# Optimization experiments

Hardware: AMD Instinct MI355X
Metric: run time of the kernel (lower is better)

## Reference

```python
import jax, jax.numpy as jnp
import numpy as np

N_GENE, N_PATH, N_VACC = 50000, 20000, 10000
N_TOT = N_GENE + N_PATH + N_VACC
HID = 128
E_PER = 250000
K_APPNP = 8
ALPHA = 0.1
N_LAYERS = 2


def setup_inputs() -> dict:
    key = jax.random.key(0)
    ks = iter(jax.random.split(key, 40))
    f32 = jnp.float32

    def nrm(shape, scale=1.0):
        return jax.random.normal(next(ks), shape, dtype=f32) * scale

    def edges(n_src, n_dst):
        src = jax.random.randint(next(ks), (E_PER,), 0, n_src)
        dst = jax.random.randint(next(ks), (E_PER,), 0, n_dst)
        return jnp.stack([src, dst]).astype(jnp.int32)

    return {
        "x_gene": nrm((N_GENE, 256)),
        "x_pathway": nrm((N_PATH, 128)),
        "x_vaccine": nrm((N_VACC, 64)),
        "win_gene": nrm((HID, 256), 256 ** -0.5),
        "bin_gene": jnp.zeros((HID,), f32),
        "win_pathway": nrm((HID, 128), 128 ** -0.5),
        "bin_pathway": jnp.zeros((HID,), f32),
        "win_vaccine": nrm((HID, 64), 64 ** -0.5),
        "bin_vaccine": jnp.zeros((HID,), f32),
        "w_sage_l": nrm((N_LAYERS, 4, HID, HID), HID ** -0.5),
        "b_sage_l": jnp.zeros((N_LAYERS, 4, HID), f32),
        "w_sage_r": nrm((N_LAYERS, 4, HID, HID), HID ** -0.5),
        "ei_targets": edges(N_VACC, N_GENE),    # vaccine -> gene
        "ei_in": edges(N_GENE, N_PATH),         # gene -> pathway
        "ei_contains": edges(N_PATH, N_GENE),   # pathway -> gene
        "ei_interacts": edges(N_GENE, N_GENE),  # gene -> gene
    }


def _sage(x_src, x_dst, ei, wl, bl, wr, n_dst):
    # PyG SAGEConv(aggr='mean'): lin_l(mean_j x_src[j]) + lin_r(x_dst); bias lives in lin_l
    src, dst = ei[0], ei[1]
    s = jax.ops.segment_sum(x_src[src], dst, num_segments=n_dst)
    cnt = jax.ops.segment_sum(jnp.ones((ei.shape[1],), x_src.dtype), dst, num_segments=n_dst)
    agg = s / jnp.maximum(cnt, 1.0)[:, None]  # isolated dst nodes -> 0
    return agg @ wl.T + bl + x_dst @ wr.T


def _forward(x_gene, x_pathway, x_vaccine, win_gene, bin_gene, win_pathway, bin_pathway,
             win_vaccine, bin_vaccine, w_sage_l, b_sage_l, w_sage_r,
             ei_targets, ei_in, ei_contains, ei_interacts):
    # input projections + relu
    hg = jax.nn.relu(x_gene @ win_gene.T + bin_gene)
    hp = jax.nn.relu(x_pathway @ win_pathway.T + bin_pathway)
    hv = jax.nn.relu(x_vaccine @ win_vaccine.T + bin_vaccine)
    # hetero SAGE layers with residual + relu (dropout: eval mode -> identity)
    for l in range(N_LAYERS):
        o_tg = _sage(hv, hg, ei_targets, w_sage_l[l, 0], b_sage_l[l, 0], w_sage_r[l, 0], N_GENE)
        o_in = _sage(hg, hp, ei_in, w_sage_l[l, 1], b_sage_l[l, 1], w_sage_r[l, 1], N_PATH)
        o_ct = _sage(hp, hg, ei_contains, w_sage_l[l, 2], b_sage_l[l, 2], w_sage_r[l, 2], N_GENE)
        o_ii = _sage(hg, hg, ei_interacts, w_sage_l[l, 3], b_sage_l[l, 3], w_sage_r[l, 3], N_GENE)
        hg = jax.nn.relu(hg + (o_tg + o_ct + o_ii) / 3.0)  # HeteroConv aggr='mean' over 3 relations
        hp = jax.nn.relu(hp + o_in)
        hv = jax.nn.relu(hv)  # no incoming relation -> zero message
    # APPNP on homogeneous graph; node order = [gene | pathway | vaccine]
    OG, OP, OV = 0, N_GENE, N_GENE + N_PATH
    loops = jnp.arange(N_TOT, dtype=jnp.int32)
    row = jnp.concatenate([ei_targets[0] + OV, ei_in[0] + OG, ei_contains[0] + OP, ei_interacts[0] + OG, loops])
    col = jnp.concatenate([ei_targets[1] + OG, ei_in[1] + OP, ei_contains[1] + OG, ei_interacts[1] + OG, loops])
    deg = jax.ops.segment_sum(jnp.ones(row.shape, hg.dtype), col, num_segments=N_TOT)
    dinv = jnp.where(deg > 0, deg ** -0.5, 0.0)
    norm = (dinv[row] * dinv[col])[:, None]
    h0 = jnp.concatenate([hg, hp, hv], axis=0)  # [N_TOT, HID]

    def step(z, _):
        m = jax.ops.segment_sum(norm * z[row], col, num_segments=N_TOT)
        return (1.0 - ALPHA) * m + ALPHA * h0, None

    z, _ = jax.lax.scan(step, h0, None, length=K_APPNP)
    return z  # [N_TOT, HID]; rows 0:50000 gene, 50000:70000 pathway, 70000:80000 vaccine


def reference(x_gene, x_pathway, x_vaccine, win_gene, bin_gene, win_pathway, bin_pathway,
              win_vaccine, bin_vaccine, w_sage_l, b_sage_l, w_sage_r,
              ei_targets, ei_in, ei_contains, ei_interacts):
    return _forward(x_gene, x_pathway, x_vaccine, win_gene, bin_gene, win_pathway, bin_pathway,
                    win_vaccine, bin_vaccine, w_sage_l, b_sage_l, w_sage_r,
                    ei_targets, ei_in, ei_contains, ei_interacts)
```

## Files before the change

### kernel.cpp

```cpp
#include <hip/hip_runtime.h>

#define N_GENE 50000
#define N_PATH 20000
#define N_VACC 10000
#define N_TOT  80000
#define HID    128
#define E_PER  250000
#define OG 0
#define OP 50000
#define OV 70000

typedef _Float16  f16x8  __attribute__((ext_vector_type(8)));
typedef _Float16  f16x4  __attribute__((ext_vector_type(4)));
typedef float     f32x4  __attribute__((ext_vector_type(4)));

__constant__ int c_segn[4] = {N_GENE, N_PATH, N_GENE, N_GENE};
__constant__ int c_segb[4] = {0, 50000, 70000, 120000};
#define CNT_TOTAL 170000

struct Off4 { int* p[4]; };
struct CntSeg { const int* dst; int* cnt; };
struct Cnt4 { CntSeg s[4]; };
struct F4Seg { const int* ei; const int* off; int* rows; int2* pk; int soff; };
struct F4 { F4Seg s[4]; };
struct AggSeg { const int* rows; const int* off; _Float16* out; int ldo; int n; };
struct Agg4 { AggSeg s[4]; };
struct CsrP { const int* off; const int2* pk; };


__global__ void count4_kernel(Cnt4 a, int* __restrict__ rank)
{
    int seg = blockIdx.y;
    int e = blockIdx.x * 256 + threadIdx.x;
    if (e < E_PER) rank[seg * E_PER + e] = atomicAdd(&a.s[seg].cnt[a.s[seg].dst[e]], 1);
}

__global__ void scan1_kernel(const int* __restrict__ cnt, int* __restrict__ partials)
{
    int seg = blockIdx.y, blk = blockIdx.x;
    int n = c_segn[seg];
    if (blk >= ((n + 4095) >> 12)) return;
    const int* base = cnt + c_segb[seg];
    int t = threadIdx.x;
    int i0 = (blk << 12) + t * 16;
    int s = 0;
#pragma unroll
    for (int j = 0; j < 16; j++) { int i = i0 + j; if (i < n) s += base[i]; }
    __shared__ int sh[256];
    sh[t] = s; __syncthreads();
    for (int d = 128; d; d >>= 1) { if (t < d) sh[t] += sh[t + d]; __syncthreads(); }
    if (t == 0) partials[seg * 32 + blk] = sh[0];
}

__global__ void scan2_kernel(int* __restrict__ partials, Off4 offs)
{
    int s = threadIdx.x;
    if (s < 4) {
        int n = c_segn[s];
        int nb = (n + 4095) >> 12;
        int run = 0;
        for (int b = 0; b < nb; b++) { int v = partials[s * 32 + b]; partials[s * 32 + b] = run; run += v; }
        offs.p[s][n] = run;
    }
}

__global__ void scan3_kernel(const int* __restrict__ cnt, const int* __restrict__ partials, Off4 offs)
{
    int seg = blockIdx.y, blk = blockIdx.x;
    int n = c_segn[seg];
    if (blk >= ((n + 4095) >> 12)) return;
    const int* base = cnt + c_segb[seg];
    int* off = offs.p[seg];
    int t = threadIdx.x;
    int i0 = (blk << 12) + t * 16;
    int loc[16];
    int s = 0;
#pragma unroll
    for (int j = 0; j < 16; j++) { int i = i0 + j; int v = (i < n) ? base[i] : 0; loc[j] = s; s += v; }
    __shared__ int sh[256];
    sh[t] = s; __syncthreads();
    for (int d = 1; d < 256; d <<= 1) {
        int v = (t >= d) ? sh[t - d] : 0; __syncthreads();
        sh[t] += v; __syncthreads();
    }
    int base_off = sh[t] - s + partials[seg * 32 + blk];
#pragma unroll
    for (int j = 0; j < 16; j++) { int i = i0 + j; if (i < n) off[i] = base_off + loc[j]; }
}

__global__ void dinv_kernel(const int* __restrict__ r0, const int* __restrict__ r1,
                            const int* __restrict__ r2, const int* __restrict__ r3,
                            float* __restrict__ dinv)
{
    int i = blockIdx.x * 256 + threadIdx.x;
    if (i >= N_TOT) return;
    int deg = 1;
    if (i < N_GENE) deg += (r0[i + 1] - r0[i]) + (r2[i + 1] - r2[i]) + (r3[i + 1] - r3[i]);
    else if (i < OV) { int k = i - OP; deg += r1[k + 1] - r1[k]; }
    dinv[i] = rsqrtf((float)deg);
}

__global__ void fill4_kernel(F4 a, const int* __restrict__ rank, const float* __restrict__ dinv)
{
    int seg = blockIdx.y;
    int e = blockIdx.x * 256 + threadIdx.x;
    if (e >= E_PER) return;
    const int* ei = a.s[seg].ei;
    int s = ei[e] + a.s[seg].soff;
    int d = ei[E_PER + e];
    int pos = a.s[seg].off[d] + rank[seg * E_PER + e];
    a.s[seg].rows[pos] = s;
    if (a.s[seg].pk) a.s[seg].pk[pos] = make_int2(s, __float_as_int(dinv[s]));
}


__global__ void agg_all_kernel(Agg4 a, const _Float16* __restrict__ Hh)
{
    int seg = blockIdx.y;
    int t = threadIdx.x;
    int node = blockIdx.x * 16 + (t >> 4);
    if (node >= a.s[seg].n) return;
    const int* rows = a.s[seg].rows;
    int sub = t & 15;
    int s = a.s[seg].off[node], e = a.s[seg].off[node + 1];
    float acc0[8] = {}, acc1[8] = {};
    int i = s;
    for (; i + 4 <= e; i += 4) {
        int r0 = rows[i], r1 = rows[i + 1], r2 = rows[i + 2], r3 = rows[i + 3];
        f16x8 x0 = *(const f16x8*)&Hh[(size_t)r0 * HID + sub * 8];
        f16x8 x1 = *(const f16x8*)&Hh[(size_t)r1 * HID + sub * 8];
        f16x8 x2 = *(const f16x8*)&Hh[(size_t)r2 * HID + sub * 8];
        f16x8 x3 = *(const f16x8*)&Hh[(size_t)r3 * HID + sub * 8];
#pragma unroll
        for (int j = 0; j < 8; j++) {
            acc0[j] += (float)x0[j] + (float)x1[j];
            acc1[j] += (float)x2[j] + (float)x3[j];
        }
    }
    for (; i < e; i++) {
        f16x8 x = *(const f16x8*)&Hh[(size_t)rows[i] * HID + sub * 8];
#pragma unroll
        for (int j = 0; j < 8; j++) acc0[j] += (float)x[j];
    }
    float inv = (e > s) ? 1.0f / (float)(e - s) : 0.0f;
    f16x8 o;
#pragma unroll
    for (int j = 0; j < 8; j++) o[j] = (_Float16)((acc0[j] + acc1[j]) * inv);
    *(f16x8*)&a.s[seg].out[(size_t)node * a.s[seg].ldo + sub * 8] = o;
}

__global__ void base_kernel(const _Float16* __restrict__ Hh, const int* __restrict__ r0rows,
                            const int* __restrict__ r0off, const float* __restrict__ dinv,
                            _Float16* __restrict__ base, _Float16* __restrict__ z0,
                            float* __restrict__ dout)
{
    int t = threadIdx.x;
    int node = blockIdx.x * 16 + (t >> 4);
    int sub = t & 15;
    size_t idx = (size_t)node * HID + sub * 8;
    f16x8 h = *(const f16x8*)&Hh[idx];
    if (node >= OV) {
        f32x4 o0, o1;
#pragma unroll
        for (int j = 0; j < 4; j++) { o0[j] = (float)h[j]; o1[j] = (float)h[j + 4]; }
        *(f32x4*)&dout[idx] = o0;
        *(f32x4*)&dout[idx + 4] = o1;
        return;
    }
    float acc[8] = {};
    if (node < N_GENE) {
        for (int i = r0off[node]; i < r0off[node + 1]; i++) {
            f16x8 v = *(const f16x8*)&Hh[(size_t)r0rows[i] * HID + sub * 8];
#pragma unroll
            for (int j = 0; j < 8; j++) acc[j] += (float)v[j];
        }
        float sc = 0.9f * dinv[node];
#pragma unroll
        for (int j = 0; j < 8; j++) acc[j] *= sc;
    }
    f16x8 bo;
#pragma unroll
    for (int j = 0; j < 8; j++) bo[j] = (_Float16)(0.1f * (float)h[j] + acc[j]);
    *(f16x8*)&base[idx] = bo;
    *(f16x8*)&z0[idx] = h;
}

__device__ __forceinline__ void gathp(const int* __restrict__ off, const int2* __restrict__ pk,
                                      int node, int sub, const _Float16* __restrict__ zin,
                                      float (&A0)[8], float (&A1)[8])
{
    int s = off[node], e = off[node + 1];
    int i = s;
    for (; i + 4 <= e; i += 4) {
        int2 p0 = pk[i], p1 = pk[i + 1], p2 = pk[i + 2], p3 = pk[i + 3];
        f16x8 x0 = *(const f16x8*)&zin[(size_t)p0.x * HID + sub * 8];
        f16x8 x1 = *(const f16x8*)&zin[(size_t)p1.x * HID + sub * 8];
        f16x8 x2 = *(const f16x8*)&zin[(size_t)p2.x * HID + sub * 8];
        f16x8 x3 = *(const f16x8*)&zin[(size_t)p3.x * HID + sub * 8];
        float w0 = __int_as_float(p0.y), w1 = __int_as_float(p1.y);
        float w2 = __int_as_float(p2.y), w3 = __int_as_float(p3.y);
#pragma unroll
        for (int j = 0; j < 8; j++) {
            A0[j] += (float)x0[j] * w0 + (float)x1[j] * w1;
            A1[j] += (float)x2[j] * w2 + (float)x3[j] * w3;
        }
    }
    for (; i < e; i++) {
        int2 p = pk[i];
        float w = __int_as_float(p.y);
        f16x8 x = *(const f16x8*)&zin[(size_t)p.x * HID + sub * 8];
#pragma unroll
        for (int j = 0; j < 8; j++) A0[j] += (float)x[j] * w;
    }
}

template<typename OT>
__launch_bounds__(256)
__global__ void appnp_kernel(const _Float16* __restrict__ zin, OT* __restrict__ zout,
                             const _Float16* __restrict__ base,
                             CsrP c1, CsrP c2, CsrP c3, const float* __restrict__ dinv)
{
    int t = threadIdx.x;
    int c = blockIdx.x * 16 + (t >> 4);
    int sub = t & 15;
    float A0[8] = {}, A1[8] = {};
    if (c < OP) {
        gathp(c2.off, c2.pk, c, sub, zin, A0, A1);
        gathp(c3.off, c3.pk, c, sub, zin, A0, A1);
    } else {
        gathp(c1.off, c1.pk, c - OP, sub, zin, A0, A1);
    }
    float dc = dinv[c];
    float d2 = dc * dc;
    size_t idx = (size_t)c * HID + sub * 8;
    f16x8 zi = *(const f16x8*)&zin[idx];
    f16x8 bs = *(const f16x8*)&base[idx];
    float res[8];
#pragma unroll
    for (int j = 0; j < 8; j++)
        res[j] = 0.9f * (dc * (A0[j] + A1[j]) + d2 * (float)zi[j]) + (float)bs[j];
    if constexpr (sizeof(OT) == 2) {
        f16x8 o;
#pragma unroll
        for (int j = 0; j < 8; j++) o[j] = (_Float16)res[j];
        *(f16x8*)&zout[idx] = o;
    } else {
        f32x4 o0, o1;
#pragma unroll
        for (int j = 0; j < 4; j++) { o0[j] = res[j]; o1[j] = res[j + 4]; }
        *(f32x4*)&zout[idx] = o0;
        *(f32x4*)&zout[idx + 4] = o1;
    }
}


__global__ void prep_all_kernel(const float* __restrict__ wg, const float* __restrict__ wp,
                                const float* __restrict__ wv,
                                _Float16* __restrict__ obg, _Float16* __restrict__ obp, _Float16* __restrict__ obv,
                                const float* __restrict__ wsl, const float* __restrict__ bsl,
                                const float* __restrict__ wsr,
                                _Float16* __restrict__ Wg0, _Float16* __restrict__ Wg1,
                                _Float16* __restrict__ Wp0, _Float16* __restrict__ Wp1,
                                float* __restrict__ bg0, float* __restrict__ bg1,
                                float* __restrict__ bp0, float* __restrict__ bp1)
{
    int y = blockIdx.y;
    int i = blockIdx.x * 256 + threadIdx.x;
    if (y == 0) {
        if (i < 32768) obg[i] = (_Float16)wg[i];
        if (i < 16384) obp[i] = (_Float16)wp[i];
        if (i < 8192)  obv[i] = (_Float16)wv[i];
        return;
    }
    int layer = y - 1;
    const float* WL = wsl + (size_t)layer * 4 * HID * HID;
    const float* WR = wsr + (size_t)layer * 4 * HID * HID;
    _Float16* Wg = layer ? Wg1 : Wg0;
    _Float16* Wp = layer ? Wp1 : Wp0;
    float* bg = layer ? bg1 : bg0;
    float* bp = layer ? bp1 : bp0;
    if (i < 128 * 512) {
        int nr = i >> 9, k = i & 511;
        float v;
        if (k < 128)      v = WL[0 * 16384 + nr * 128 + k];
        else if (k < 256) v = WL[2 * 16384 + nr * 128 + (k - 128)];
        else if (k < 384) v = WL[3 * 16384 + nr * 128 + (k - 256)];
        else {
            int kk = k - 384;
            v = WR[0 * 16384 + nr * 128 + kk] + WR[2 * 16384 + nr * 128 + kk] + WR[3 * 16384 + nr * 128 + kk];
        }
        Wg[i] = (_Float16)v;
    }
    if (i < 128 * 256) {
        int nr = i >> 8, k = i & 255;
        float v = (k < 128) ? WL[1 * 16384 + nr * 128 + k] : WR[1 * 16384 + nr * 128 + (k - 128)];
        Wp[i] = (_Float16)v;
    }
    if (i < 128) {
        const float* BL = bsl + (size_t)layer * 4 * HID;
        bg[i] = BL[0 * 128 + i] + BL[2 * 128 + i] + BL[3 * 128 + i];
        bp[i] = BL[1 * 128 + i];
    }
}


template<int KT, int K1, bool A_F32, bool SAGE>
__launch_bounds__(256)
__global__ void tgemm_kernel(const void* __restrict__ A1_, const _Float16* __restrict__ A2,
                             const _Float16* __restrict__ W, const float* __restrict__ bias,
                             float scale, _Float16* __restrict__ Hh, int M)
{
    __shared__ _Float16 lds[128 * 40];
    int t = threadIdx.x;
    int wave = t >> 6, lane = t & 63;
    int r = lane & 15, quad = lane >> 4;
    int mbase = blockIdx.x * 128 + wave * 32;
    int mm0 = min(mbase + r, M - 1);
    int mm1 = min(mbase + 16 + r, M - 1);
    const float* Af = (const float*)A1_;
    const _Float16* Ab = (const _Float16*)A1_;

    f32x4 acc[2][8];
#pragma unroll
    for (int s = 0; s < 2; s++)
#pragma unroll
        for (int n = 0; n < 8; n++) acc[s][n] = (f32x4){0.f, 0.f, 0.f, 0.f};

    int srow = t >> 1;
    int selt = (t & 1) * 16;

#pragma unroll
    for (int k0 = 0; k0 < KT; k0 += 32) {
        __syncthreads();
        {
            const _Float16* wsrc = W + (size_t)srow * KT + k0 + selt;
            f16x8 w0 = *(const f16x8*)wsrc;
            f16x8 w1 = *(const f16x8*)(wsrc + 8);
            *(f16x8*)&lds[srow * 40 + selt] = w0;
            *(f16x8*)&lds[srow * 40 + selt + 8] = w1;
        }
        f16x8 a0, a1;
        if constexpr (A_F32) {
            const float* p0 = Af + (size_t)mm0 * KT + k0 + quad * 8;
            const float* p1 = Af + (size_t)mm1 * KT + k0 + quad * 8;
            f32x4 x0 = *(const f32x4*)p0, x1 = *(const f32x4*)(p0 + 4);
            f32x4 y0 = *(const f32x4*)p1, y1 = *(const f32x4*)(p1 + 4);
#pragma unroll
            for (int j = 0; j < 4; j++) { a0[j] = (_Float16)x0[j]; a0[j + 4] = (_Float16)x1[j]; }
#pragma unroll
            for (int j = 0; j < 4; j++) { a1[j] = (_Float16)y0[j]; a1[j + 4] = (_Float16)y1[j]; }
        } else if (k0 < K1) {
            a0 = *(const f16x8*)(Ab + (size_t)mm0 * K1 + k0 + quad * 8);
            a1 = *(const f16x8*)(Ab + (size_t)mm1 * K1 + k0 + quad * 8);
        } else {
            a0 = *(const f16x8*)(A2 + (size_t)mm0 * 128 + (k0 - K1) + quad * 8);
            a1 = *(const f16x8*)(A2 + (size_t)mm1 * 128 + (k0 - K1) + quad * 8);
        }
        __syncthreads();
#pragma unroll
        for (int nt = 0; nt < 8; nt++) {
            f16x8 b = *(const f16x8*)&lds[(nt * 16 + r) * 40 + quad * 8];
            acc[0][nt] = __builtin_amdgcn_mfma_f32_16x16x32_f16(a0, b, acc[0][nt], 0, 0, 0);
            acc[1][nt] = __builtin_amdgcn_mfma_f32_16x16x32_f16(a1, b, acc[1][nt], 0, 0, 0);
        }
    }

#pragma unroll
    for (int sub = 0; sub < 2; sub++) {
#pragma unroll
        for (int nt = 0; nt < 8; nt++) {
            int n = nt * 16 + r;
            float bv = bias[n];
#pragma unroll
            for (int i = 0; i < 4; i++) {
                int row = mbase + sub * 16 + quad * 4 + i;
                if (row >= M) continue;
                size_t idx = (size_t)row * HID + n;
                float v;
                if constexpr (SAGE) v = fmaxf((float)Hh[idx] + (acc[sub][nt][i] + bv) * scale, 0.f);
                else                v = fmaxf(acc[sub][nt][i] + bv, 0.f);
                Hh[idx] = (_Float16)v;
            }
        }
    }
}


extern "C" void kernel_launch(void* const* d_in, const int* in_sizes, int n_in,
                              void* d_out, int out_size, void* d_ws, size_t ws_size,
                              hipStream_t stream)
{
    (void)in_sizes; (void)n_in; (void)out_size; (void)ws_size;

    const float* x_gene = (const float*)d_in[0];
    const float* x_path = (const float*)d_in[1];
    const float* x_vacc = (const float*)d_in[2];
    const float* win_g  = (const float*)d_in[3];
    const float* bin_g  = (const float*)d_in[4];
    const float* win_p  = (const float*)d_in[5];
    const float* bin_p  = (const float*)d_in[6];
    const float* win_v  = (const float*)d_in[7];
    const float* bin_v  = (const float*)d_in[8];
    const float* wsl    = (const float*)d_in[9];
    const float* bsl    = (const float*)d_in[10];
    const float* wsr    = (const float*)d_in[11];
    const int* ei_tg  = (const int*)d_in[12];
    const int* ei_ing = (const int*)d_in[13];
    const int* ei_ct  = (const int*)d_in[14];
    const int* ei_ii  = (const int*)d_in[15];

    char* p = (char*)d_ws;
    auto alloc = [&](size_t b) { char* r = p; p += (b + 255) & ~((size_t)255); return r; };

    _Float16* Hh   = (_Float16*)alloc((size_t)N_TOT * HID * 2);
    _Float16* BASE = (_Float16*)alloc((size_t)OV * HID * 2);
    _Float16* Z1   = (_Float16*)alloc((size_t)OV * HID * 2);
    _Float16* Z2   = (_Float16*)alloc((size_t)OV * HID * 2);
    _Float16* AGG_G = (_Float16*)alloc((size_t)N_GENE * 384 * 2);
    _Float16* AGG_P = (_Float16*)alloc((size_t)N_PATH * 128 * 2);
    float* dinv   = (float*)alloc((size_t)N_TOT * 4);
    int* r_rows[4], *r_off[4];
    for (int r = 0; r < 4; r++) r_rows[r] = (int*)alloc((size_t)E_PER * 4);
    r_off[0] = (int*)alloc((size_t)(N_GENE + 1) * 4);
    r_off[1] = (int*)alloc((size_t)(N_PATH + 1) * 4);
    r_off[2] = (int*)alloc((size_t)(N_GENE + 1) * 4);
    r_off[3] = (int*)alloc((size_t)(N_GENE + 1) * 4);
    int2* pk1 = (int2*)alloc((size_t)E_PER * 8);
    int2* pk2 = (int2*)alloc((size_t)E_PER * 8);
    int2* pk3 = (int2*)alloc((size_t)E_PER * 8);
    int* rank = (int*)alloc((size_t)4 * E_PER * 4);
    int* partials = (int*)alloc((size_t)4 * 32 * 4);
    _Float16* wh_g = (_Float16*)alloc((size_t)HID * 256 * 2);
    _Float16* wh_p = (_Float16*)alloc((size_t)HID * 128 * 2);
    _Float16* wh_v = (_Float16*)alloc((size_t)HID * 64 * 2);
    _Float16* Wg[2]; _Float16* Wp[2]; float* bg[2]; float* bp[2];
    for (int l = 0; l < 2; l++) {
        Wg[l] = (_Float16*)alloc((size_t)128 * 512 * 2);
        Wp[l] = (_Float16*)alloc((size_t)128 * 256 * 2);
        bg[l] = (float*)alloc(128 * 4);
        bp[l] = (float*)alloc(128 * 4);
    }
    char* zb = p;
    int* cnt = (int*)alloc((size_t)CNT_TOTAL * 4);
    hipMemsetAsync(zb, 0, (size_t)(p - zb), stream);

    Off4 offs;
    offs.p[0] = r_off[0]; offs.p[1] = r_off[1]; offs.p[2] = r_off[2]; offs.p[3] = r_off[3];

    const int GE = (E_PER + 255) / 256;
    const int TB_G = (N_GENE + 127) / 128;
    const int TB_P = (N_PATH + 127) / 128;
    const int TB_V = (N_VACC + 127) / 128;

    prep_all_kernel<<<dim3(256, 3), 256, 0, stream>>>(win_g, win_p, win_v, wh_g, wh_p, wh_v,
                                                      wsl, bsl, wsr, Wg[0], Wg[1], Wp[0], Wp[1],
                                                      bg[0], bg[1], bp[0], bp[1]);

    Cnt4 c4;
    c4.s[0] = {ei_tg + E_PER,  cnt + 0};
    c4.s[1] = {ei_ing + E_PER, cnt + 50000};
    c4.s[2] = {ei_ct + E_PER,  cnt + 70000};
    c4.s[3] = {ei_ii + E_PER,  cnt + 120000};
    count4_kernel<<<dim3(GE, 4), 256, 0, stream>>>(c4, rank);

    dim3 sg((N_GENE + 4095) / 4096, 4);
    scan1_kernel<<<sg, 256, 0, stream>>>(cnt, partials);
    scan2_kernel<<<1, 64, 0, stream>>>(partials, offs);
    scan3_kernel<<<sg, 256, 0, stream>>>(cnt, partials, offs);

    dinv_kernel<<<(N_TOT + 255) / 256, 256, 0, stream>>>(r_off[0], r_off[1], r_off[2], r_off[3], dinv);

    F4 f4;
    f4.s[0] = {ei_tg,  r_off[0], r_rows[0], nullptr, OV};
    f4.s[1] = {ei_ing, r_off[1], r_rows[1], pk1,     OG};
    f4.s[2] = {ei_ct,  r_off[2], r_rows[2], pk2,     OP};
    f4.s[3] = {ei_ii,  r_off[3], r_rows[3], pk3,     OG};
    fill4_kernel<<<dim3(GE, 4), 256, 0, stream>>>(f4, rank, dinv);

    tgemm_kernel<256, 256, true, false><<<TB_G, 256, 0, stream>>>(x_gene, nullptr, wh_g, bin_g, 1.f, Hh, N_GENE);
    tgemm_kernel<128, 128, true, false><<<TB_P, 256, 0, stream>>>(x_path, nullptr, wh_p, bin_p, 1.f,
                                                                  Hh + (size_t)OP * HID, N_PATH);
    tgemm_kernel< 64,  64, true, false><<<TB_V, 256, 0, stream>>>(x_vacc, nullptr, wh_v, bin_v, 1.f,
                                                                  Hh + (size_t)OV * HID, N_VACC);

    for (int l = 0; l < 2; l++) {
        Agg4 ag;
        ag.s[0] = {r_rows[0], r_off[0], AGG_G + 0,   384, N_GENE};
        ag.s[1] = {r_rows[2], r_off[2], AGG_G + 128, 384, N_GENE};
        ag.s[2] = {r_rows[3], r_off[3], AGG_G + 256, 384, N_GENE};
        ag.s[3] = {r_rows[1], r_off[1], AGG_P,       128, N_PATH};
        agg_all_kernel<<<dim3((N_GENE + 15) / 16, 4), 256, 0, stream>>>(ag, Hh);

        tgemm_kernel<512, 384, false, true><<<TB_G, 256, 0, stream>>>(AGG_G, Hh, Wg[l], bg[l],
                                                                      1.0f / 3.0f, Hh, N_GENE);
        tgemm_kernel<256, 128, false, true><<<TB_P, 256, 0, stream>>>(AGG_P, Hh + (size_t)OP * HID, Wp[l], bp[l],
                                                                      1.0f, Hh + (size_t)OP * HID, N_PATH);
    }

    float* dout = (float*)d_out;
    base_kernel<<<N_TOT / 16, 256, 0, stream>>>(Hh, r_rows[0], r_off[0], dinv, BASE, Z1, dout);

    CsrP c1 = {r_off[1], pk1};
    CsrP c2 = {r_off[2], pk2};
    CsrP c3 = {r_off[3], pk3};
    const int GA = OV / 16;
    appnp_kernel<<<GA, 256, 0, stream>>>(Z1, Z2, BASE, c1, c2, c3, dinv);
    appnp_kernel<<<GA, 256, 0, stream>>>(Z2, Z1, BASE, c1, c2, c3, dinv);
    appnp_kernel<<<GA, 256, 0, stream>>>(Z1, Z2, BASE, c1, c2, c3, dinv);
    appnp_kernel<<<GA, 256, 0, stream>>>(Z2, Z1, BASE, c1, c2, c3, dinv);
    appnp_kernel<<<GA, 256, 0, stream>>>(Z1, Z2, BASE, c1, c2, c3, dinv);
    appnp_kernel<<<GA, 256, 0, stream>>>(Z2, Z1, BASE, c1, c2, c3, dinv);
    appnp_kernel<<<GA, 256, 0, stream>>>(Z1, Z2, BASE, c1, c2, c3, dinv);
    appnp_kernel<<<GA, 256, 0, stream>>>(Z2, dout, BASE, c1, c2, c3, dinv);
}
```

Before: 723.3 us.

## Merge gene CSR edge lists and use 8 lanes per node for gathers

Builds one merged CSR (moff/pkG) for gene destinations by interleaving the contains and interacts edge lists per node, so each APPNP step walks a single contiguous neighbour range instead of two. Separately, the aggregation, base and APPNP kernels now use 8 threads per node, each loading two 16-byte chunks, so 32 nodes fit in a block instead of 16. This is meant to cut loop overhead and per-node offset loads and to raise memory-level parallelism per thread. The cost is more registers per thread and a slightly more complex fill step.

```diff
diff --git a/kernel.cpp b/kernel.cpp
--- a/kernel.cpp
+++ b/kernel.cpp
@@ -11,7 +11,6 @@
 #define OV 70000
 
 typedef _Float16  f16x8  __attribute__((ext_vector_type(8)));
-typedef _Float16  f16x4  __attribute__((ext_vector_type(4)));
 typedef float     f32x4  __attribute__((ext_vector_type(4)));
 
 __constant__ int c_segn[4] = {N_GENE, N_PATH, N_GENE, N_GENE};
@@ -90,7 +89,7 @@
 
 __global__ void dinv_kernel(const int* __restrict__ r0, const int* __restrict__ r1,
                             const int* __restrict__ r2, const int* __restrict__ r3,
-                            float* __restrict__ dinv)
+                            float* __restrict__ dinv, int* __restrict__ moff)
 {
     int i = blockIdx.x * 256 + threadIdx.x;
     if (i >= N_TOT) return;
@@ -98,9 +97,11 @@
     if (i < N_GENE) deg += (r0[i + 1] - r0[i]) + (r2[i + 1] - r2[i]) + (r3[i + 1] - r3[i]);
     else if (i < OV) { int k = i - OP; deg += r1[k + 1] - r1[k]; }
     dinv[i] = rsqrtf((float)deg);
-}
-
-__global__ void fill4_kernel(F4 a, const int* __restrict__ rank, const float* __restrict__ dinv)
+    if (i <= N_GENE) moff[i] = r2[i] + r3[i];
+}
+
+__global__ void fill4_kernel(F4 a, const int* __restrict__ rank, const float* __restrict__ dinv,
+                             int2* __restrict__ pkG)
 {
     int seg = blockIdx.y;
     int e = blockIdx.x * 256 + threadIdx.x;
@@ -108,9 +109,18 @@
     const int* ei = a.s[seg].ei;
     int s = ei[e] + a.s[seg].soff;
     int d = ei[E_PER + e];
-    int pos = a.s[seg].off[d] + rank[seg * E_PER + e];
+    int rk = rank[seg * E_PER + e];
+    int pos = a.s[seg].off[d] + rk;
     a.s[seg].rows[pos] = s;
-    if (a.s[seg].pk) a.s[seg].pk[pos] = make_int2(s, __float_as_int(dinv[s]));
+    if (seg == 1) {
+        a.s[1].pk[pos] = make_int2(s, __float_as_int(dinv[s]));
+    } else if (seg == 2) {
+        int mpos = pos + a.s[3].off[d];
+        pkG[mpos] = make_int2(s, __float_as_int(dinv[s]));
+    } else if (seg == 3) {
+        int mpos = pos + a.s[2].off[d + 1];
+        pkG[mpos] = make_int2(s, __float_as_int(dinv[s]));
+    }
 }
 
 
@@ -118,35 +128,42 @@
 {
     int seg = blockIdx.y;
     int t = threadIdx.x;
-    int node = blockIdx.x * 16 + (t >> 4);
+    int node = blockIdx.x * 32 + (t >> 3);
     if (node >= a.s[seg].n) return;
+    int o0 = (t & 7) * 8;
     const int* rows = a.s[seg].rows;
-    int sub = t & 15;
     int s = a.s[seg].off[node], e = a.s[seg].off[node + 1];
-    float acc0[8] = {}, acc1[8] = {};
+    float A[16] = {};
     int i = s;
     for (; i + 4 <= e; i += 4) {
         int r0 = rows[i], r1 = rows[i + 1], r2 = rows[i + 2], r3 = rows[i + 3];
-        f16x8 x0 = *(const f16x8*)&Hh[(size_t)r0 * HID + sub * 8];
-        f16x8 x1 = *(const f16x8*)&Hh[(size_t)r1 * HID + sub * 8];
-        f16x8 x2 = *(const f16x8*)&Hh[(size_t)r2 * HID + sub * 8];
-        f16x8 x3 = *(const f16x8*)&Hh[(size_t)r3 * HID + sub * 8];
+        const _Float16* b0 = &Hh[(size_t)r0 * HID + o0];
+        const _Float16* b1 = &Hh[(size_t)r1 * HID + o0];
+        const _Float16* b2 = &Hh[(size_t)r2 * HID + o0];
+        const _Float16* b3 = &Hh[(size_t)r3 * HID + o0];
+        f16x8 x0a = *(const f16x8*)b0, x0b = *(const f16x8*)(b0 + 64);
+        f16x8 x1a = *(const f16x8*)b1, x1b = *(const f16x8*)(b1 + 64);
+        f16x8 x2a = *(const f16x8*)b2, x2b = *(const f16x8*)(b2 + 64);
+        f16x8 x3a = *(const f16x8*)b3, x3b = *(const f16x8*)(b3 + 64);
 #pragma unroll
         for (int j = 0; j < 8; j++) {
-            acc0[j] += (float)x0[j] + (float)x1[j];
-            acc1[j] += (float)x2[j] + (float)x3[j];
+            A[j]     += ((float)x0a[j] + (float)x1a[j]) + ((float)x2a[j] + (float)x3a[j]);
+            A[j + 8] += ((float)x0b[j] + (float)x1b[j]) + ((float)x2b[j] + (float)x3b[j]);
         }
     }
     for (; i < e; i++) {
-        f16x8 x = *(const f16x8*)&Hh[(size_t)rows[i] * HID + sub * 8];
-#pragma unroll
-        for (int j = 0; j < 8; j++) acc0[j] += (float)x[j];
+        const _Float16* b = &Hh[(size_t)rows[i] * HID + o0];
+        f16x8 xa = *(const f16x8*)b, xb = *(const f16x8*)(b + 64);
+#pragma unroll
+        for (int j = 0; j < 8; j++) { A[j] += (float)xa[j]; A[j + 8] += (float)xb[j]; }
     }
     float inv = (e > s) ? 1.0f / (float)(e - s) : 0.0f;
-    f16x8 o;
-#pragma unroll
-    for (int j = 0; j < 8; j++) o[j] = (_Float16)((acc0[j] + acc1[j]) * inv);
-    *(f16x8*)&a.s[seg].out[(size_t)node * a.s[seg].ldo + sub * 8] = o;
+    f16x8 oa, ob;
+#pragma unroll
+    for (int j = 0; j < 8; j++) { oa[j] = (_Float16)(A[j] * inv); ob[j] = (_Float16)(A[j + 8] * inv); }
+    _Float16* out = a.s[seg].out + (size_t)node * a.s[seg].ldo + o0;
+    *(f16x8*)out = oa;
+    *(f16x8*)(out + 64) = ob;
 }
 
 __global__ void base_kernel(const _Float16* __restrict__ Hh, const int* __restrict__ r0rows,
@@ -155,62 +172,92 @@
                             float* __restrict__ dout)
 {
     int t = threadIdx.x;
-    int node = blockIdx.x * 16 + (t >> 4);
-    int sub = t & 15;
-    size_t idx = (size_t)node * HID + sub * 8;
-    f16x8 h = *(const f16x8*)&Hh[idx];
+    int node = blockIdx.x * 32 + (t >> 3);
+    int o0 = (t & 7) * 8;
+    size_t i0 = (size_t)node * HID + o0;
+    size_t i1 = i0 + 64;
+    f16x8 ha = *(const f16x8*)&Hh[i0];
+    f16x8 hb = *(const f16x8*)&Hh[i1];
     if (node >= OV) {
-        f32x4 o0, o1;
-#pragma unroll
-        for (int j = 0; j < 4; j++) { o0[j] = (float)h[j]; o1[j] = (float)h[j + 4]; }
-        *(f32x4*)&dout[idx] = o0;
-        *(f32x4*)&dout[idx + 4] = o1;
+        f32x4 oa0, oa1, ob0, ob1;
+#pragma unroll
+        for (int j = 0; j < 4; j++) {
+            oa0[j] = (float)ha[j]; oa1[j] = (float)ha[j + 4];
+            ob0[j] = (float)hb[j]; ob1[j] = (float)hb[j + 4];
+        }
+        *(f32x4*)&dout[i0] = oa0; *(f32x4*)&dout[i0 + 4] = oa1;
+        *(f32x4*)&dout[i1] = ob0; *(f32x4*)&dout[i1 + 4] = ob1;
         return;
     }
-    float acc[8] = {};
+    float A[16] = {};
     if (node < N_GENE) {
-        for (int i = r0off[node]; i < r0off[node + 1]; i++) {
-            f16x8 v = *(const f16x8*)&Hh[(size_t)r0rows[i] * HID + sub * 8];
-#pragma unroll
-            for (int j = 0; j < 8; j++) acc[j] += (float)v[j];
+        int s = r0off[node], e = r0off[node + 1];
+        int i = s;
+        for (; i + 4 <= e; i += 4) {
+            int r0 = r0rows[i], r1 = r0rows[i + 1], r2 = r0rows[i + 2], r3 = r0rows[i + 3];
+            const _Float16* b0 = &Hh[(size_t)r0 * HID + o0];
+            const _Float16* b1 = &Hh[(size_t)r1 * HID + o0];
+            const _Float16* b2 = &Hh[(size_t)r2 * HID + o0];
+            const _Float16* b3 = &Hh[(size_t)r3 * HID + o0];
+            f16x8 x0a = *(const f16x8*)b0, x0b = *(const f16x8*)(b0 + 64);
+            f16x8 x1a = *(const f16x8*)b1, x1b = *(const f16x8*)(b1 + 64);
+            f16x8 x2a = *(const f16x8*)b2, x2b = *(const f16x8*)(b2 + 64);
+            f16x8 x3a = *(const f16x8*)b3, x3b = *(const f16x8*)(b3 + 64);
+#pragma unroll
+            for (int j = 0; j < 8; j++) {
+                A[j]     += ((float)x0a[j] + (float)x1a[j]) + ((float)x2a[j] + (float)x3a[j]);
+                A[j + 8] += ((float)x0b[j] + (float)x1b[j]) + ((float)x2b[j] + (float)x3b[j]);
+            }
+        }
+        for (; i < e; i++) {
+            const _Float16* b = &Hh[(size_t)r0rows[i] * HID + o0];
+            f16x8 xa = *(const f16x8*)b, xb = *(const f16x8*)(b + 64);
+#pragma unroll
+            for (int j = 0; j < 8; j++) { A[j] += (float)xa[j]; A[j + 8] += (float)xb[j]; }
         }
         float sc = 0.9f * dinv[node];
 #pragma unroll
-        for (int j = 0; j < 8; j++) acc[j] *= sc;
-    }
-    f16x8 bo;
-#pragma unroll
-    for (int j = 0; j < 8; j++) bo[j] = (_Float16)(0.1f * (float)h[j] + acc[j]);
-    *(f16x8*)&base[idx] = bo;
-    *(f16x8*)&z0[idx] = h;
-}
-
-__device__ __forceinline__ void gathp(const int* __restrict__ off, const int2* __restrict__ pk,
-                                      int node, int sub, const _Float16* __restrict__ zin,
-                                      float (&A0)[8], float (&A1)[8])
-{
-    int s = off[node], e = off[node + 1];
+        for (int j = 0; j < 16; j++) A[j] *= sc;
+    }
+    f16x8 ba, bb;
+#pragma unroll
+    for (int j = 0; j < 8; j++) {
+        ba[j] = (_Float16)(0.1f * (float)ha[j] + A[j]);
+        bb[j] = (_Float16)(0.1f * (float)hb[j] + A[j + 8]);
+    }
+    *(f16x8*)&base[i0] = ba; *(f16x8*)&base[i1] = bb;
+    *(f16x8*)&z0[i0] = ha;   *(f16x8*)&z0[i1] = hb;
+}
+
+__device__ __forceinline__ void gath8(const int2* __restrict__ pk, int s, int e, int o0,
+                                      const _Float16* __restrict__ zin, float (&A)[16])
+{
     int i = s;
     for (; i + 4 <= e; i += 4) {
         int2 p0 = pk[i], p1 = pk[i + 1], p2 = pk[i + 2], p3 = pk[i + 3];
-        f16x8 x0 = *(const f16x8*)&zin[(size_t)p0.x * HID + sub * 8];
-        f16x8 x1 = *(const f16x8*)&zin[(size_t)p1.x * HID + sub * 8];
-        f16x8 x2 = *(const f16x8*)&zin[(size_t)p2.x * HID + sub * 8];
-        f16x8 x3 = *(const f16x8*)&zin[(size_t)p3.x * HID + sub * 8];
+        const _Float16* b0 = &zin[(size_t)p0.x * HID + o0];
+        const _Float16* b1 = &zin[(size_t)p1.x * HID + o0];
+        const _Float16* b2 = &zin[(size_t)p2.x * HID + o0];
+        const _Float16* b3 = &zin[(size_t)p3.x * HID + o0];
+        f16x8 x0a = *(const f16x8*)b0, x0b = *(const f16x8*)(b0 + 64);
+        f16x8 x1a = *(const f16x8*)b1, x1b = *(const f16x8*)(b1 + 64);
+        f16x8 x2a = *(const f16x8*)b2, x2b = *(const f16x8*)(b2 + 64);
+        f16x8 x3a = *(const f16x8*)b3, x3b = *(const f16x8*)(b3 + 64);
         float w0 = __int_as_float(p0.y), w1 = __int_as_float(p1.y);
         float w2 = __int_as_float(p2.y), w3 = __int_as_float(p3.y);
 #pragma unroll
         for (int j = 0; j < 8; j++) {
-            A0[j] += (float)x0[j] * w0 + (float)x1[j] * w1;
-            A1[j] += (float)x2[j] * w2 + (float)x3[j] * w3;
+            A[j]     += ((float)x0a[j] * w0 + (float)x1a[j] * w1) + ((float)x2a[j] * w2 + (float)x3a[j] * w3);
+            A[j + 8] += ((float)x0b[j] * w0 + (float)x1b[j] * w1) + ((float)x2b[j] * w2 + (float)x3b[j] * w3);
         }
     }
     for (; i < e; i++) {
         int2 p = pk[i];
+        const _Float16* b = &zin[(size_t)p.x * HID + o0];
+        f16x8 xa = *(const f16x8*)b, xb = *(const f16x8*)(b + 64);
         float w = __int_as_float(p.y);
-        f16x8 x = *(const f16x8*)&zin[(size_t)p.x * HID + sub * 8];
-#pragma unroll
-        for (int j = 0; j < 8; j++) A0[j] += (float)x[j] * w;
+#pragma unroll
+        for (int j = 0; j < 8; j++) { A[j] += (float)xa[j] * w; A[j + 8] += (float)xb[j] * w; }
     }
 }
 
@@ -218,38 +265,47 @@
 __launch_bounds__(256)
 __global__ void appnp_kernel(const _Float16* __restrict__ zin, OT* __restrict__ zout,
                              const _Float16* __restrict__ base,
-                             CsrP c1, CsrP c2, CsrP c3, const float* __restrict__ dinv)
+                             const int* __restrict__ moff, const int2* __restrict__ pkG,
+                             CsrP c1, const float* __restrict__ dinv)
 {
     int t = threadIdx.x;
-    int c = blockIdx.x * 16 + (t >> 4);
-    int sub = t & 15;
-    float A0[8] = {}, A1[8] = {};
+    int c = blockIdx.x * 32 + (t >> 3);
+    if (c >= OV) return;
+    int o0 = (t & 7) * 8;
+    float A[16] = {};
     if (c < OP) {
-        gathp(c2.off, c2.pk, c, sub, zin, A0, A1);
-        gathp(c3.off, c3.pk, c, sub, zin, A0, A1);
+        gath8(pkG, moff[c], moff[c + 1], o0, zin, A);
     } else {
-        gathp(c1.off, c1.pk, c - OP, sub, zin, A0, A1);
+        int k = c - OP;
+        gath8(c1.pk, c1.off[k], c1.off[k + 1], o0, zin, A);
     }
     float dc = dinv[c];
     float d2 = dc * dc;
-    size_t idx = (size_t)c * HID + sub * 8;
-    f16x8 zi = *(const f16x8*)&zin[idx];
-    f16x8 bs = *(const f16x8*)&base[idx];
-    float res[8];
-#pragma unroll
-    for (int j = 0; j < 8; j++)
-        res[j] = 0.9f * (dc * (A0[j] + A1[j]) + d2 * (float)zi[j]) + (float)bs[j];
+    size_t i0 = (size_t)c * HID + o0;
+    size_t i1 = i0 + 64;
+    f16x8 za = *(const f16x8*)&zin[i0], zb = *(const f16x8*)&zin[i1];
+    f16x8 ba = *(const f16x8*)&base[i0], bb = *(const f16x8*)&base[i1];
+    float ra[8], rb[8];
+#pragma unroll
+    for (int j = 0; j < 8; j++) {
+        ra[j] = 0.9f * (dc * A[j]     + d2 * (float)za[j]) + (float)ba[j];
+        rb[j] = 0.9f * (dc * A[j + 8] + d2 * (float)zb[j]) + (float)bb[j];
+    }
     if constexpr (sizeof(OT) == 2) {
-        f16x8 o;
-#pragma unroll
-        for (int j = 0; j < 8; j++) o[j] = (_Float16)res[j];
-        *(f16x8*)&zout[idx] = o;
+        f16x8 oa, ob;
+#pragma unroll
+        for (int j = 0; j < 8; j++) { oa[j] = (_Float16)ra[j]; ob[j] = (_Float16)rb[j]; }
+        *(f16x8*)&zout[i0] = oa;
+        *(f16x8*)&zout[i1] = ob;
     } else {
-        f32x4 o0, o1;
-#pragma unroll
-        for (int j = 0; j < 4; j++) { o0[j] = res[j]; o1[j] = res[j + 4]; }
-        *(f32x4*)&zout[idx] = o0;
-        *(f32x4*)&zout[idx + 4] = o1;
+        f32x4 oa0, oa1, ob0, ob1;
+#pragma unroll
+        for (int j = 0; j < 4; j++) {
+            oa0[j] = ra[j]; oa1[j] = ra[j + 4];
+            ob0[j] = rb[j]; ob1[j] = rb[j + 4];
+        }
+        *(f32x4*)&zout[i0] = oa0; *(f32x4*)&zout[i0 + 4] = oa1;
+        *(f32x4*)&zout[i1] = ob0; *(f32x4*)&zout[i1 + 4] = ob1;
     }
 }
 
@@ -425,9 +481,9 @@
     r_off[1] = (int*)alloc((size_t)(N_PATH + 1) * 4);
     r_off[2] = (int*)alloc((size_t)(N_GENE + 1) * 4);
     r_off[3] = (int*)alloc((size_t)(N_GENE + 1) * 4);
+    int* moff = (int*)alloc((size_t)(N_GENE + 1) * 4);
     int2* pk1 = (int2*)alloc((size_t)E_PER * 8);
-    int2* pk2 = (int2*)alloc((size_t)E_PER * 8);
-    int2* pk3 = (int2*)alloc((size_t)E_PER * 8);
+    int2* pkG = (int2*)alloc((size_t)2 * E_PER * 8);
     int* rank = (int*)alloc((size_t)4 * E_PER * 4);
     int* partials = (int*)alloc((size_t)4 * 32 * 4);
     _Float16* wh_g = (_Float16*)alloc((size_t)HID * 256 * 2);
@@ -468,14 +524,14 @@
     scan2_kernel<<<1, 64, 0, stream>>>(partials, offs);
     scan3_kernel<<<sg, 256, 0, stream>>>(cnt, partials, offs);
 
-    dinv_kernel<<<(N_TOT + 255) / 256, 256, 0, stream>>>(r_off[0], r_off[1], r_off[2], r_off[3], dinv);
+    dinv_kernel<<<(N_TOT + 255) / 256, 256, 0, stream>>>(r_off[0], r_off[1], r_off[2], r_off[3], dinv, moff);
 
     F4 f4;
     f4.s[0] = {ei_tg,  r_off[0], r_rows[0], nullptr, OV};
     f4.s[1] = {ei_ing, r_off[1], r_rows[1], pk1,     OG};
-    f4.s[2] = {ei_ct,  r_off[2], r_rows[2], pk2,     OP};
-    f4.s[3] = {ei_ii,  r_off[3], r_rows[3], pk3,     OG};
-    fill4_kernel<<<dim3(GE, 4), 256, 0, stream>>>(f4, rank, dinv);
+    f4.s[2] = {ei_ct,  r_off[2], r_rows[2], nullptr, OP};
+    f4.s[3] = {ei_ii,  r_off[3], r_rows[3], nullptr, OG};
+    fill4_kernel<<<dim3(GE, 4), 256, 0, stream>>>(f4, rank, dinv, pkG);
 
     tgemm_kernel<256, 256, true, false><<<TB_G, 256, 0, stream>>>(x_gene, nullptr, wh_g, bin_g, 1.f, Hh, N_GENE);
     tgemm_kernel<128, 128, true, false><<<TB_P, 256, 0, stream>>>(x_path, nullptr, wh_p, bin_p, 1.f,
@@ -489,7 +545,7 @@
         ag.s[1] = {r_rows[2], r_off[2], AGG_G + 128, 384, N_GENE};
         ag.s[2] = {r_rows[3], r_off[3], AGG_G + 256, 384, N_GENE};
         ag.s[3] = {r_rows[1], r_off[1], AGG_P,       128, N_PATH};
-        agg_all_kernel<<<dim3((N_GENE + 15) / 16, 4), 256, 0, stream>>>(ag, Hh);
+        agg_all_kernel<<<dim3((N_GENE + 31) / 32, 4), 256, 0, stream>>>(ag, Hh);
 
         tgemm_kernel<512, 384, false, true><<<TB_G, 256, 0, stream>>>(AGG_G, Hh, Wg[l], bg[l],
                                                                       1.0f / 3.0f, Hh, N_GENE);
@@ -498,18 +554,16 @@
     }
 
     float* dout = (float*)d_out;
-    base_kernel<<<N_TOT / 16, 256, 0, stream>>>(Hh, r_rows[0], r_off[0], dinv, BASE, Z1, dout);
+    base_kernel<<<N_TOT / 32, 256, 0, stream>>>(Hh, r_rows[0], r_off[0], dinv, BASE, Z1, dout);
 
     CsrP c1 = {r_off[1], pk1};
-    CsrP c2 = {r_off[2], pk2};
-    CsrP c3 = {r_off[3], pk3};
-    const int GA = OV / 16;
-    appnp_kernel<<<GA, 256, 0, stream>>>(Z1, Z2, BASE, c1, c2, c3, dinv);
-    appnp_kernel<<<GA, 256, 0, stream>>>(Z2, Z1, BASE, c1, c2, c3, dinv);
-    appnp_kernel<<<GA, 256, 0, stream>>>(Z1, Z2, BASE, c1, c2, c3, dinv);
-    appnp_kernel<<<GA, 256, 0, stream>>>(Z2, Z1, BASE, c1, c2, c3, dinv);
-    appnp_kernel<<<GA, 256, 0, stream>>>(Z1, Z2, BASE, c1, c2, c3, dinv);
-    appnp_kernel<<<GA, 256, 0, stream>>>(Z2, Z1, BASE, c1, c2, c3, dinv);
-    appnp_kernel<<<GA, 256, 0, stream>>>(Z1, Z2, BASE, c1, c2, c3, dinv);
-    appnp_kernel<<<GA, 256, 0, stream>>>(Z2, dout, BASE, c1, c2, c3, dinv);
-}
+    const int GA = (OV + 31) / 32;
+    appnp_kernel<<<GA, 256, 0, stream>>>(Z1, Z2, BASE, moff, pkG, c1, dinv);
+    appnp_kernel<<<GA, 256, 0, stream>>>(Z2, Z1, BASE, moff, pkG, c1, dinv);
+    appnp_kernel<<<GA, 256, 0, stream>>>(Z1, Z2, BASE, moff, pkG, c1, dinv);
+    appnp_kernel<<<GA, 256, 0, stream>>>(Z2, Z1, BASE, moff, pkG, c1, dinv);
+    appnp_kernel<<<GA, 256, 0, stream>>>(Z1, Z2, BASE, moff, pkG, c1, dinv);
+    appnp_kernel<<<GA, 256, 0, stream>>>(Z2, Z1, BASE, moff, pkG, c1, dinv);
+    appnp_kernel<<<GA, 256, 0, stream>>>(Z1, Z2, BASE, moff, pkG, c1, dinv);
+    appnp_kernel<<<GA, 256, 0, stream>>>(Z2, dout, BASE, moff, pkG, c1, dinv);
+}
```

Measured after the change: 734.8 us. About the same (+1.6%).
